# Kernel tuning notes

Hardware: AMD Instinct MI355X
Metric: run time of the kernel (lower is better)

Reference implementation:

```python
import jax, jax.numpy as jnp
import numpy as np

B, N, C, H = 8, 2048, 1024, 16
D = C // H
FOCUSING_FACTOR = 3
KERNEL = 5
EPS_BN = 1e-5


def setup_inputs() -> dict:
    key = jax.random.key(0)
    ks = jax.random.split(key, 6)
    s = lambda k, shape: jax.random.normal(k, shape, dtype=jnp.float32) * 0.02
    return {
        "hidden_states": jax.random.normal(ks[0], (B, N, C), dtype=jnp.float32),
        "bn_gamma": jnp.ones((C,), jnp.float32),
        "bn_beta": jnp.zeros((C,), jnp.float32),
        "W_qkv": s(ks[1], (C, 3 * C)),
        "b_qkv": jnp.zeros((3 * C,), jnp.float32),
        "scale_p": jnp.zeros((1, 1, C), jnp.float32),
        "dwc_w": s(ks[2], (C, 1, KERNEL)),
        "dwc_b": jnp.zeros((C,), jnp.float32),
        "W_proj": s(ks[3], (C, C)),
        "b_proj": jnp.zeros((C,), jnp.float32),
    }


def _focus(t, scale):
    # Focused feature map: relu kernel, scale, then power-3 sharpening with norm restoration
    t = jax.nn.relu(t) + 1e-6
    t = t / scale
    nrm = jnp.linalg.norm(t, axis=-1, keepdims=True)
    t = t ** FOCUSING_FACTOR
    return t / jnp.linalg.norm(t, axis=-1, keepdims=True) * nrm


def reference(hidden_states, bn_gamma, bn_beta, W_qkv, b_qkv, scale_p, dwc_w, dwc_b, W_proj, b_proj):
    x = hidden_states  # (B, N, C)
    # BatchNorm1d in training mode: per-channel stats over batch and sequence
    mean = jnp.mean(x, axis=(0, 1))
    var = jnp.mean((x - mean) ** 2, axis=(0, 1))  # biased, as torch BN uses
    xn = (x - mean) * jax.lax.rsqrt(var + EPS_BN) * bn_gamma + bn_beta

    qkv = xn @ W_qkv + b_qkv
    q, k, v = jnp.split(qkv, 3, axis=-1)
    scale = jax.nn.softplus(scale_p)
    q = _focus(q, scale)
    k = _focus(k, scale)

    heads = lambda t: t.reshape(B, N, H, D).transpose(0, 2, 1, 3)  # (B,H,N,D)
    qh, kh, vh = heads(q), heads(k), heads(v)

    # Linear attention: O(N*D^2) instead of O(N^2*D)
    z = 1.0 / (jnp.einsum('bhnd,bhd->bhn', qh, kh.sum(axis=2)) + 1e-6)
    kv = jnp.einsum('bhnd,bhne->bhde', kh, vh)  # (B,H,D,D)
    o = jnp.einsum('bhnd,bhde->bhne', qh, kv) * z[..., None]
    o = o.transpose(0, 2, 1, 3).reshape(B, N, C)

    # Depthwise conv residual on v over the sequence dim
    vc = v.transpose(0, 2, 1)  # (B,C,N)
    dwc = jax.lax.conv_general_dilated(
        vc, dwc_w, window_strides=(1,), padding=[(KERNEL // 2, KERNEL // 2)],
        dimension_numbers=('NCH', 'OIH', 'NCH'), feature_group_count=C)
    dwc = (dwc + dwc_b[None, :, None]).transpose(0, 2, 1)

    return (o + dwc) @ W_proj + b_proj
```

## Files before the change

### kernel.cpp

```cpp
#include <hip/hip_runtime.h>


#define DEV __device__ __forceinline__

typedef __attribute__((ext_vector_type(8))) short bf16x8;
typedef __attribute__((ext_vector_type(4))) float f32x4;
typedef unsigned short us;

DEV float bf2f(us u) {
  union { unsigned int i; float f; } v; v.i = ((unsigned int)u) << 16; return v.f;
}
DEV us f2bf(float f) {
  union { float f; unsigned int i; } v; v.f = f;
  unsigned int r = v.i + 0x7FFFu + ((v.i >> 16) & 1u);
  return (us)(r >> 16);
}
DEV void glds16(const us* g, us* l) {
  __builtin_amdgcn_global_load_lds((const __attribute__((address_space(1))) unsigned int*)g,
                                   (__attribute__((address_space(3))) unsigned int*)l, 16, 0, 0);
}

#define MEMFENCE asm volatile("" ::: "memory")

__global__ void zero_f32(float* p, int n) {
  int i = blockIdx.x * 256 + threadIdx.x;
  if (i < n) p[i] = 0.f;
}

__global__ __launch_bounds__(256) void bn_stats(const float* __restrict__ x,
                                                float* __restrict__ s_sum, float* __restrict__ s_sq) {
  int t = threadIdx.x;
  int c0 = t * 4;
  size_t row0 = (size_t)blockIdx.x * 64;
  float s[4] = {0.f,0.f,0.f,0.f}, q[4] = {0.f,0.f,0.f,0.f};
  for (int r = 0; r < 64; ++r) {
    f32x4 v = *(const f32x4*)&x[(row0 + r) * 1024 + c0];
    #pragma unroll
    for (int i = 0; i < 4; ++i) { float f = v[i]; s[i] += f; q[i] += f * f; }
  }
  #pragma unroll
  for (int i = 0; i < 4; ++i) { atomicAdd(&s_sum[c0 + i], s[i]); atomicAdd(&s_sq[c0 + i], q[i]); }
}

__global__ void bn_finalize(const float* __restrict__ s_sum, const float* __restrict__ s_sq,
                            const float* __restrict__ gamma, const float* __restrict__ beta,
                            const float* __restrict__ scalep,
                            float* __restrict__ bn_a, float* __restrict__ bn_b, float* __restrict__ invs) {
  int c = threadIdx.x;
  float mean = s_sum[c] * (1.0f / 16384.0f);
  float var  = s_sq[c] * (1.0f / 16384.0f) - mean * mean;
  float a = gamma[c] * rsqrtf(var + 1e-5f);
  bn_a[c] = a;
  bn_b[c] = beta[c] - mean * a;
  float sv = scalep[c];
  float sp = (sv > 20.f) ? sv : log1pf(expf(sv));
  invs[c] = 1.0f / sp;
}

__global__ __launch_bounds__(256) void xn_to_bf16(const float* __restrict__ x,
                                                  const float* __restrict__ bn_a, const float* __restrict__ bn_b,
                                                  us* __restrict__ xn) {
  size_t base = ((size_t)blockIdx.x * 256 + threadIdx.x) * 8;
  int c = (int)(base & 1023);
  f32x4 a0 = *(const f32x4*)&x[base];
  f32x4 a1 = *(const f32x4*)&x[base + 4];
  uint4 o; us* uo = (us*)&o;
  #pragma unroll
  for (int i = 0; i < 4; ++i) uo[i] = f2bf(bn_a[c + i] * a0[i] + bn_b[c + i]);
  #pragma unroll
  for (int i = 0; i < 4; ++i) uo[4 + i] = f2bf(bn_a[c + 4 + i] * a1[i] + bn_b[c + 4 + i]);
  *(uint4*)&xn[base] = o;
}

__global__ __launch_bounds__(256) void transpose_f32_bf16(const float* __restrict__ in,
                                                          us* __restrict__ out, int R, int Cc) {
  __shared__ float tile[64 * 65];
  int tx = blockIdx.x * 64, ty = blockIdx.y * 64;
  int t = threadIdx.x;
  {
    int rr = t >> 4, g = t & 15;
    #pragma unroll
    for (int p = 0; p < 4; ++p) {
      int r = p * 16 + rr;
      f32x4 v = *(const f32x4*)&in[(size_t)(ty + r) * Cc + tx + g * 4];
      #pragma unroll
      for (int i = 0; i < 4; ++i) tile[r * 65 + g * 4 + i] = v[i];
    }
  }
  __syncthreads();
  {
    int rr = t >> 3, g = t & 7;
    #pragma unroll
    for (int p = 0; p < 2; ++p) {
      int nl = p * 32 + rr;
      uint4 v; us* u = (us*)&v;
      #pragma unroll
      for (int j = 0; j < 8; ++j) u[j] = f2bf(tile[(g * 8 + j) * 65 + nl]);
      *(uint4*)&out[(size_t)(tx + nl) * R + ty + g * 8] = v;
    }
  }
}

template <typename OutT>
__global__ __launch_bounds__(512, 2) void gemm256(const us* __restrict__ A,
                                                  const us* __restrict__ Bt,
                                                  const float* __restrict__ bias,
                                                  OutT* __restrict__ Ca,
                                                  OutT* __restrict__ Cb) {
  constexpr int GK = 1024;
  __shared__ __align__(16) us As[2][256 * 64];
  __shared__ __align__(16) us Bs[2][256 * 64];
  int t = threadIdx.x;
  int wid = t >> 6, lane = t & 63;
  int l16 = lane & 15, qd = lane >> 4;
  int nwx = gridDim.x;
  int id = blockIdx.y * nwx + blockIdx.x;
  int nwg = nwx * (int)gridDim.y;
  int sw = (id & 7) * (nwg >> 3) + (id >> 3);
  int n0 = (sw % nwx) * 256, m0 = (sw / nwx) * 256;

  int rr = lane >> 3, lg = (lane & 7) ^ rr;
  const us* Abase = A + (size_t)(m0 + wid * 32 + rr) * GK + lg * 8;
  const us* Bbase = Bt + (size_t)(n0 + wid * 32 + rr) * GK + lg * 8;
  us* lA = (us*)&As[0][0] + (wid * 32) * 64;
  us* lB = (us*)&Bs[0][0] + (wid * 32) * 64;

  int wr = wid >> 2, wc = wid & 3;

  f32x4 acc[8][4];
  const f32x4 zero4 = {0.f, 0.f, 0.f, 0.f};
  #pragma unroll
  for (int i = 0; i < 8; ++i)
    #pragma unroll
    for (int j = 0; j < 4; ++j) acc[i][j] = zero4;

  auto STAGE = [&](int kt) {
    int b = kt & 1;
    const us* sa = Abase + kt * 64;
    const us* sb = Bbase + kt * 64;
    #pragma unroll
    for (int g = 0; g < 4; ++g) {
      glds16(sa + (size_t)g * 8 * GK, lA + b * 16384 + g * 8 * 64);
      glds16(sb + (size_t)g * 8 * GK, lB + b * 16384 + g * 8 * 64);
    }
  };

  auto BODY = [&](int kt) {
    int b = kt & 1;
    #pragma unroll
    for (int ks = 0; ks < 2; ++ks) {
      bf16x8 af[8], bfr[4];
      #pragma unroll
      for (int i = 0; i < 8; ++i) {
        int r = wr * 128 + i * 16 + l16;
        int sl = (ks * 4 + qd) ^ (r & 7);
        af[i] = *(const bf16x8*)&As[b][r * 64 + sl * 8];
      }
      #pragma unroll
      for (int j = 0; j < 4; ++j) {
        int r = wc * 64 + j * 16 + l16;
        int sl = (ks * 4 + qd) ^ (r & 7);
        bfr[j] = *(const bf16x8*)&Bs[b][r * 64 + sl * 8];
      }
      __builtin_amdgcn_s_setprio(1);
      #pragma unroll
      for (int i = 0; i < 8; ++i)
        #pragma unroll
        for (int j = 0; j < 4; ++j)
          acc[i][j] = __builtin_amdgcn_mfma_f32_16x16x32_bf16(af[i], bfr[j], acc[i][j], 0, 0, 0);
      __builtin_amdgcn_s_setprio(0);
    }
  };

  STAGE(0);
  asm volatile("s_waitcnt vmcnt(0)" ::: "memory");
  MEMFENCE; __builtin_amdgcn_s_barrier(); MEMFENCE;

  for (int kt = 0; kt < 16; ++kt) {
    if (kt + 1 < 16) STAGE(kt + 1);
    BODY(kt);
    if (kt + 1 < 16) {
      asm volatile("s_waitcnt vmcnt(0)" ::: "memory");
      MEMFENCE; __builtin_amdgcn_s_barrier(); MEMFENCE;
    }
  }

  OutT* Cp; int col0;
  if (n0 < 1024) { Cp = Ca; col0 = n0; } else { Cp = Cb; col0 = n0 - 1024; }
  #pragma unroll
  for (int i = 0; i < 8; ++i) {
    int row = m0 + wr * 128 + i * 16 + qd * 4;
    #pragma unroll
    for (int j = 0; j < 4; ++j) {
      int fc = n0 + wc * 64 + j * 16 + l16;
      float bv = bias[fc];
      int col = col0 + wc * 64 + j * 16 + l16;
      #pragma unroll
      for (int r = 0; r < 4; ++r) {
        float val = acc[i][j][r] + bv;
        if constexpr (sizeof(OutT) == 2)
          ((us*)Cp)[(size_t)(row + r) * 1024 + col] = f2bf(val);
        else
          ((float*)Cp)[(size_t)(row + r) * 1024 + col] = val;
      }
    }
  }
}

__global__ __launch_bounds__(256) void focus_kernel(us* __restrict__ buf,
                                                    const float* __restrict__ invs) {
  int row = blockIdx.x;
  us* p = buf + (size_t)row * 1024;
  int t = threadIdx.x;
  int c0 = t * 4;
  uint2 v = *(uint2*)&p[c0];
  us* u = (us*)&v;
  float ti[4]; float s2 = 0.f, s6 = 0.f;
  #pragma unroll
  for (int i = 0; i < 4; ++i) {
    float f = bf2f(u[i]);
    f = fmaxf(f, 0.f) + 1e-6f;
    f *= invs[c0 + i];
    ti[i] = f;
    float f2 = f * f;
    s2 += f2; s6 += f2 * f2 * f2;
  }
  #pragma unroll
  for (int off = 32; off > 0; off >>= 1) { s2 += __shfl_down(s2, off); s6 += __shfl_down(s6, off); }
  __shared__ float red[8]; __shared__ float bc;
  int wid = t >> 6, lane = t & 63;
  if (lane == 0) { red[wid] = s2; red[4 + wid] = s6; }
  __syncthreads();
  if (t == 0) {
    float a = red[0] + red[1] + red[2] + red[3];
    float b2 = red[4] + red[5] + red[6] + red[7];
    bc = sqrtf(a / b2);
  }
  __syncthreads();
  float factor = bc;
  #pragma unroll
  for (int i = 0; i < 4; ++i) u[i] = f2bf(ti[i] * ti[i] * ti[i] * factor);
  *(uint2*)&p[c0] = v;
}

__global__ __launch_bounds__(256) void attn_stats3(const us* __restrict__ kbuf,
                                                   const us* __restrict__ vbuf,
                                                   float* __restrict__ ksum,
                                                   float* __restrict__ kvpart) {
  int cx = blockIdx.x, h = blockIdx.y, b = blockIdx.z, bh = b * 16 + h;
  int t = threadIdx.x, wid = t >> 6, lane = t & 63;
  int l16 = lane & 15, qd = lane >> 4;
  int wm = (wid & 1) * 32, wn = (wid >> 1) * 32;
  __shared__ __align__(16) us kT[64 * 80];
  __shared__ __align__(16) us vT[64 * 80];
  const f32x4 zero4 = {0.f, 0.f, 0.f, 0.f};
  f32x4 acc[2][2];
  #pragma unroll
  for (int i = 0; i < 2; ++i)
    #pragma unroll
    for (int j = 0; j < 2; ++j) acc[i][j] = zero4;
  float ksacc = 0.f;
  int np = (t & 31) * 2, ch0 = (t >> 5) * 8;

  for (int ck = 0; ck < 4; ++ck) {
    __syncthreads();
    size_t base = ((size_t)b * 2048 + cx * 256 + ck * 64 + np) * 1024 + h * 64 + ch0;
    uint4 k0 = *(const uint4*)&kbuf[base];
    uint4 k1 = *(const uint4*)&kbuf[base + 1024];
    uint4 v0 = *(const uint4*)&vbuf[base];
    uint4 v1 = *(const uint4*)&vbuf[base + 1024];
    us* pk0 = (us*)&k0; us* pk1 = (us*)&k1; us* pv0 = (us*)&v0; us* pv1 = (us*)&v1;
    #pragma unroll
    for (int i = 0; i < 8; ++i) {
      unsigned int pk = (unsigned int)pk0[i] | ((unsigned int)pk1[i] << 16);
      unsigned int pv = (unsigned int)pv0[i] | ((unsigned int)pv1[i] << 16);
      *(unsigned int*)&kT[(ch0 + i) * 80 + np] = pk;
      *(unsigned int*)&vT[(ch0 + i) * 80 + np] = pv;
    }
    __syncthreads();
    if (t < 64) {
      #pragma unroll
      for (int g = 0; g < 8; ++g) {
        bf16x8 kk = *(const bf16x8*)&kT[t * 80 + g * 8];
        #pragma unroll
        for (int j = 0; j < 8; ++j) ksacc += bf2f(((us*)&kk)[j]);
      }
    }
    #pragma unroll
    for (int ks = 0; ks < 2; ++ks) {
      bf16x8 af[2], bfr[2];
      #pragma unroll
      for (int i = 0; i < 2; ++i) {
        af[i]  = *(const bf16x8*)&kT[(wm + i * 16 + l16) * 80 + ks * 32 + qd * 8];
        bfr[i] = *(const bf16x8*)&vT[(wn + i * 16 + l16) * 80 + ks * 32 + qd * 8];
      }
      #pragma unroll
      for (int i = 0; i < 2; ++i)
        #pragma unroll
        for (int j = 0; j < 2; ++j)
          acc[i][j] = __builtin_amdgcn_mfma_f32_16x16x32_bf16(af[i], bfr[j], acc[i][j], 0, 0, 0);
    }
  }
  float* pp = kvpart + ((size_t)cx * 128 + bh) * 4096;
  #pragma unroll
  for (int i = 0; i < 2; ++i) {
    int d = wm + i * 16 + qd * 4;
    #pragma unroll
    for (int j = 0; j < 2; ++j) {
      int e = wn + j * 16 + l16;
      #pragma unroll
      for (int r = 0; r < 4; ++r) pp[(d + r) * 64 + e] = acc[i][j][r];
    }
  }
  if (t < 64) atomicAdd(&ksum[bh * 64 + t], ksacc);
}

__global__ __launch_bounds__(256) void kv_reduce(const float* __restrict__ part, us* __restrict__ kvT) {
  int bh = blockIdx.x;
  int t = threadIdx.x;
  __shared__ float kvl[4096];
  #pragma unroll
  for (int p = 0; p < 16; ++p) {
    int i = p * 256 + t;
    float s = 0.f;
    #pragma unroll
    for (int c = 0; c < 8; ++c) s += part[((size_t)c * 128 + bh) * 4096 + i];
    kvl[i] = s;
  }
  __syncthreads();
  #pragma unroll
  for (int p = 0; p < 2; ++p) {
    int idx = p * 256 + t;
    int e = idx >> 3, d0 = (idx & 7) * 8;
    uint4 o; us* uo = (us*)&o;
    #pragma unroll
    for (int i = 0; i < 8; ++i) uo[i] = f2bf(kvl[(d0 + i) * 64 + e]);
    *(uint4*)&kvT[(size_t)bh * 4096 + e * 64 + d0] = o;
  }
}

__global__ __launch_bounds__(256) void attn_o2(us* __restrict__ qod,
                                               const us* __restrict__ vbuf,
                                               const float* __restrict__ ksum,
                                               const us* __restrict__ kvT,
                                               const float* __restrict__ dwcw,
                                               const float* __restrict__ dwcb) {
  int nt = blockIdx.x, h = blockIdx.y, b = blockIdx.z, bh = b * 16 + h;
  int t = threadIdx.x, wid = t >> 6, lane = t & 63;
  int l16 = lane & 15, qd = lane >> 4;
  __shared__ __align__(16) us qs[128 * 64];
  __shared__ __align__(16) us bs[64 * 64];
  __shared__ __align__(16) us vs[132 * 64];
  __shared__ float zl[128];
  __shared__ float ksl[64];
  __shared__ float wl[64 * 5];
  __shared__ float bl[64];
  int rS = t >> 3, gS = t & 7;
  size_t qbase = ((size_t)b * 2048 + nt * 128) * 1024 + h * 64;
  #pragma unroll
  for (int p = 0; p < 4; ++p) {
    int r = p * 32 + rS;
    uint4 v = *(const uint4*)&qod[qbase + (size_t)r * 1024 + gS * 8];
    *(uint4*)&qs[r * 64 + ((gS ^ (r & 7)) * 8)] = v;
  }
  #pragma unroll
  for (int p = 0; p < 2; ++p) {
    int r = p * 32 + rS;
    uint4 v = *(const uint4*)&kvT[(size_t)bh * 4096 + r * 64 + gS * 8];
    *(uint4*)&bs[r * 64 + ((gS ^ (r & 7)) * 8)] = v;
  }
  int n0 = nt * 128;
  #pragma unroll
  for (int p = 0; p < 5; ++p) {
    int idx = p * 256 + t;
    if (idx < 1056) {
      int r = idx >> 3, g = idx & 7;
      int n = n0 - 2 + r;
      uint4 v = make_uint4(0, 0, 0, 0);
      if (n >= 0 && n < 2048)
        v = *(const uint4*)&vbuf[((size_t)b * 2048 + n) * 1024 + h * 64 + g * 8];
      *(uint4*)&vs[r * 64 + g * 8] = v;
    }
  }
  if (t < 64) {
    ksl[t] = ksum[bh * 64 + t];
    bl[t] = dwcb[h * 64 + t];
    #pragma unroll
    for (int j = 0; j < 5; ++j) wl[t * 5 + j] = dwcw[(h * 64 + t) * 5 + j];
  }
  __syncthreads();
  if (t < 128) {
    float zs = 0.f;
    #pragma unroll
    for (int g = 0; g < 8; ++g) {
      bf16x8 qv = *(const bf16x8*)&qs[t * 64 + ((g ^ (t & 7)) * 8)];
      #pragma unroll
      for (int j = 0; j < 8; ++j) zs += bf2f(((us*)&qv)[j]) * ksl[g * 8 + j];
    }
    zl[t] = 1.f / (zs + 1e-6f);
  }
  __syncthreads();
  const f32x4 zero4 = {0.f, 0.f, 0.f, 0.f};
  f32x4 acc[2][4];
  #pragma unroll
  for (int i = 0; i < 2; ++i)
    #pragma unroll
    for (int j = 0; j < 4; ++j) acc[i][j] = zero4;
  #pragma unroll
  for (int ks = 0; ks < 2; ++ks) {
    bf16x8 af[2], bfr[4];
    #pragma unroll
    for (int i = 0; i < 2; ++i) {
      int ml = (wid * 2 + i) * 16 + l16;
      af[i] = *(const bf16x8*)&qs[ml * 64 + (((ks * 4 + qd) ^ (ml & 7)) * 8)];
    }
    #pragma unroll
    for (int j = 0; j < 4; ++j) {
      int nl = j * 16 + l16;
      bfr[j] = *(const bf16x8*)&bs[nl * 64 + (((ks * 4 + qd) ^ (nl & 7)) * 8)];
    }
    #pragma unroll
    for (int i = 0; i < 2; ++i)
      #pragma unroll
      for (int j = 0; j < 4; ++j)
        acc[i][j] = __builtin_amdgcn_mfma_f32_16x16x32_bf16(af[i], bfr[j], acc[i][j], 0, 0, 0);
  }
  #pragma unroll
  for (int i = 0; i < 2; ++i) {
    int rl0 = (wid * 2 + i) * 16 + qd * 4;
    #pragma unroll
    for (int j = 0; j < 4; ++j) {
      int e = j * 16 + l16;
      float w0 = wl[e * 5], w1 = wl[e * 5 + 1], w2 = wl[e * 5 + 2], w3 = wl[e * 5 + 3], w4 = wl[e * 5 + 4];
      float vv[8];
      #pragma unroll
      for (int m = 0; m < 8; ++m) vv[m] = bf2f(vs[(rl0 + m) * 64 + e]);
      float bb = bl[e];
      #pragma unroll
      for (int r = 0; r < 4; ++r) {
        float dwc = vv[r] * w0 + vv[r + 1] * w1 + vv[r + 2] * w2 + vv[r + 3] * w3 + vv[r + 4] * w4;
        float o = acc[i][j][r] * zl[rl0 + r] + dwc + bb;
        qod[qbase + (size_t)(rl0 + r) * 1024 + e] = f2bf(o);
      }
    }
  }
}

extern "C" void kernel_launch(void* const* d_in, const int* in_sizes, int n_in,
                              void* d_out, int out_size, void* d_ws, size_t ws_size,
                              hipStream_t stream) {
  const float* x      = (const float*)d_in[0];
  const float* gamma  = (const float*)d_in[1];
  const float* beta   = (const float*)d_in[2];
  const float* Wqkv   = (const float*)d_in[3];
  const float* bqkv   = (const float*)d_in[4];
  const float* scalep = (const float*)d_in[5];
  const float* dwcw   = (const float*)d_in[6];
  const float* dwcb   = (const float*)d_in[7];
  const float* Wproj  = (const float*)d_in[8];
  const float* bproj  = (const float*)d_in[9];
  float* out = (float*)d_out;

  float* wsf = (float*)d_ws;
  float* s_sum  = wsf;
  float* s_sq   = wsf + 1024;
  float* ksum   = wsf + 2048;
  float* bn_a   = wsf + 10240;
  float* bn_b   = wsf + 11264;
  float* invs   = wsf + 12288;
  float* kvpart = wsf + 13312;
  us* kvT = (us*)(wsf + 4207616);
  us* wtq = (us*)(wsf + 4469760);
  us* wtp = (us*)(wsf + 6042624);
  us* kq  = (us*)(wsf + 6566912);
  us* vbf = (us*)d_out;
  us* xnb = (us*)d_out + 16777216;

  zero_f32<<<40, 256, 0, stream>>>(wsf, 10240);
  bn_stats<<<256, 256, 0, stream>>>(x, s_sum, s_sq);
  bn_finalize<<<1, 1024, 0, stream>>>(s_sum, s_sq, gamma, beta, scalep, bn_a, bn_b, invs);
  xn_to_bf16<<<8192, 256, 0, stream>>>(x, bn_a, bn_b, xnb);
  transpose_f32_bf16<<<dim3(48, 16), 256, 0, stream>>>(Wqkv, wtq, 1024, 3072);
  transpose_f32_bf16<<<dim3(16, 16), 256, 0, stream>>>(Wproj, wtp, 1024, 1024);

  gemm256<us><<<dim3(8, 64), 512, 0, stream>>>(xnb, wtq + 1024 * 1024, bqkv + 1024, kq, vbf);
  focus_kernel<<<16384, 256, 0, stream>>>(kq, invs);
  attn_stats3<<<dim3(8, 16, 8), 256, 0, stream>>>(kq, vbf, ksum, kvpart);
  kv_reduce<<<128, 256, 0, stream>>>(kvpart, kvT);
  gemm256<us><<<dim3(4, 64), 512, 0, stream>>>(xnb, wtq, bqkv, kq, kq);
  focus_kernel<<<16384, 256, 0, stream>>>(kq, invs);
  attn_o2<<<dim3(16, 16, 8), 256, 0, stream>>>(kq, vbf, ksum, kvT, dwcw, dwcb);
  gemm256<float><<<dim3(4, 64), 512, 0, stream>>>(kq, wtp, bproj, out, out);
}
```

Baseline: 409.9 us.

## Restructure GEMM main loop into barrier-phased interleaved loads and MFMA

Splits each K-tile of the 256x256 bf16 GEMM into four phases. Each phase loads a half set of A fragments (plus B fragments where needed) from LDS, issues part of the next tile's global-to-LDS copy, then runs 16 MFMAs between workgroup barriers. The LDS layout changes to two 128-row halves per operand, and staging rows are interleaved across waves. The goal is to overlap global loads and LDS reads with matrix math, in the style of a ping-pong schedule, at the cost of many more barriers per iteration.

```diff
diff --git a/kernel.cpp b/kernel.cpp
--- a/kernel.cpp
+++ b/kernel.cpp
@@ -21,6 +21,8 @@
 }
 
 #define MEMFENCE asm volatile("" ::: "memory")
+#define BAR do { MEMFENCE; __builtin_amdgcn_s_barrier(); MEMFENCE; } while (0)
+#define LGKM0 asm volatile("s_waitcnt lgkmcnt(0)" ::: "memory")
 
 __global__ void zero_f32(float* p, int n) {
   int i = blockIdx.x * 256 + threadIdx.x;
@@ -108,8 +110,8 @@
                                                   OutT* __restrict__ Ca,
                                                   OutT* __restrict__ Cb) {
   constexpr int GK = 1024;
-  __shared__ __align__(16) us As[2][256 * 64];
-  __shared__ __align__(16) us Bs[2][256 * 64];
+  __shared__ __align__(16) us As[2][2][128 * 64];
+  __shared__ __align__(16) us Bs[2][2][128 * 64];
   int t = threadIdx.x;
   int wid = t >> 6, lane = t & 63;
   int l16 = lane & 15, qd = lane >> 4;
@@ -120,12 +122,11 @@
   int n0 = (sw % nwx) * 256, m0 = (sw / nwx) * 256;
 
   int rr = lane >> 3, lg = (lane & 7) ^ rr;
-  const us* Abase = A + (size_t)(m0 + wid * 32 + rr) * GK + lg * 8;
-  const us* Bbase = Bt + (size_t)(n0 + wid * 32 + rr) * GK + lg * 8;
-  us* lA = (us*)&As[0][0] + (wid * 32) * 64;
-  us* lB = (us*)&Bs[0][0] + (wid * 32) * 64;
+  const us* Asrc = A + (size_t)(m0 + wid * 8 + rr) * GK + lg * 8;
+  const us* Bsrc = Bt + (size_t)(n0 + wid * 8 + rr) * GK + lg * 8;
 
   int wr = wid >> 2, wc = wid & 3;
+  int bh = wc >> 1, brow0 = (wc & 1) * 64;
 
   f32x4 acc[8][4];
   const f32x4 zero4 = {0.f, 0.f, 0.f, 0.f};
@@ -134,55 +135,64 @@
     #pragma unroll
     for (int j = 0; j < 4; ++j) acc[i][j] = zero4;
 
-  auto STAGE = [&](int kt) {
-    int b = kt & 1;
-    const us* sa = Abase + kt * 64;
-    const us* sb = Bbase + kt * 64;
-    #pragma unroll
-    for (int g = 0; g < 4; ++g) {
-      glds16(sa + (size_t)g * 8 * GK, lA + b * 16384 + g * 8 * 64);
-      glds16(sb + (size_t)g * 8 * GK, lB + b * 16384 + g * 8 * 64);
-    }
+  auto STAGE_A = [&](int kt, int b) {
+    const us* src = Asrc + kt * 64;
+    us* dst = (us*)&As[b][0][0] + wid * 512;
+    #pragma unroll
+    for (int g = 0; g < 4; ++g)
+      glds16(src + (size_t)(g * 64) * GK, dst + g * 4096);
   };
-
-  auto BODY = [&](int kt) {
-    int b = kt & 1;
-    #pragma unroll
-    for (int ks = 0; ks < 2; ++ks) {
-      bf16x8 af[8], bfr[4];
-      #pragma unroll
-      for (int i = 0; i < 8; ++i) {
-        int r = wr * 128 + i * 16 + l16;
-        int sl = (ks * 4 + qd) ^ (r & 7);
-        af[i] = *(const bf16x8*)&As[b][r * 64 + sl * 8];
-      }
-      #pragma unroll
-      for (int j = 0; j < 4; ++j) {
-        int r = wc * 64 + j * 16 + l16;
-        int sl = (ks * 4 + qd) ^ (r & 7);
-        bfr[j] = *(const bf16x8*)&Bs[b][r * 64 + sl * 8];
-      }
-      __builtin_amdgcn_s_setprio(1);
-      #pragma unroll
-      for (int i = 0; i < 8; ++i)
-        #pragma unroll
-        for (int j = 0; j < 4; ++j)
-          acc[i][j] = __builtin_amdgcn_mfma_f32_16x16x32_bf16(af[i], bfr[j], acc[i][j], 0, 0, 0);
-      __builtin_amdgcn_s_setprio(0);
-    }
+  auto STAGE_B = [&](int kt, int b) {
+    const us* src = Bsrc + kt * 64;
+    us* dst = (us*)&Bs[b][0][0] + wid * 512;
+    #pragma unroll
+    for (int g = 0; g < 4; ++g)
+      glds16(src + (size_t)(g * 64) * GK, dst + g * 4096);
   };
-
-  STAGE(0);
+  auto LDA = [&](bf16x8* dst, int i0, int ks, int b) {
+    #pragma unroll
+    for (int i = 0; i < 4; ++i) {
+      int r = (i0 + i) * 16 + l16;
+      int sl = (ks * 4 + qd) ^ (r & 7);
+      dst[i] = *(const bf16x8*)&As[b][wr][r * 64 + sl * 8];
+    }
+  };
+  auto LDB = [&](bf16x8* dst, int ks, int b) {
+    #pragma unroll
+    for (int j = 0; j < 4; ++j) {
+      int r = brow0 + j * 16 + l16;
+      int sl = (ks * 4 + qd) ^ (r & 7);
+      dst[j] = *(const bf16x8*)&Bs[b][bh][r * 64 + sl * 8];
+    }
+  };
+  auto MM = [&](int i0, bf16x8* a4, bf16x8* b4) {
+    __builtin_amdgcn_s_setprio(1);
+    #pragma unroll
+    for (int i = 0; i < 4; ++i)
+      #pragma unroll
+      for (int j = 0; j < 4; ++j)
+        acc[i0 + i][j] = __builtin_amdgcn_mfma_f32_16x16x32_bf16(a4[i], b4[j], acc[i0 + i][j], 0, 0, 0);
+    __builtin_amdgcn_s_setprio(0);
+  };
+
+  STAGE_A(0, 0); STAGE_B(0, 0);
   asm volatile("s_waitcnt vmcnt(0)" ::: "memory");
-  MEMFENCE; __builtin_amdgcn_s_barrier(); MEMFENCE;
+  BAR;
 
   for (int kt = 0; kt < 16; ++kt) {
-    if (kt + 1 < 16) STAGE(kt + 1);
-    BODY(kt);
-    if (kt + 1 < 16) {
-      asm volatile("s_waitcnt vmcnt(0)" ::: "memory");
-      MEMFENCE; __builtin_amdgcn_s_barrier(); MEMFENCE;
-    }
+    int buf = kt & 1, nxt = buf ^ 1;
+    bf16x8 afl[4], afh[4], bfv[4];
+    LDA(afl, 0, 0, buf); LDB(bfv, 0, buf);
+    if (kt < 15) STAGE_A(kt + 1, nxt);
+    BAR; LGKM0; MM(0, afl, bfv); BAR;
+    LDA(afh, 4, 0, buf);
+    if (kt < 15) STAGE_B(kt + 1, nxt);
+    BAR; LGKM0; MM(4, afh, bfv); BAR;
+    LDA(afl, 0, 1, buf); LDB(bfv, 1, buf);
+    BAR; LGKM0; MM(0, afl, bfv); BAR;
+    LDA(afh, 4, 1, buf);
+    asm volatile("s_waitcnt vmcnt(0)" ::: "memory");
+    BAR; LGKM0; MM(4, afh, bfv); BAR;
   }
 
   OutT* Cp; int col0;
```

After: 397.1 us. 3.1% less time.
